# Kernel tuning notes

Hardware: AMD Instinct MI355X
Metric: run time of the kernel (lower is better)

Reference implementation:

```python
import jax, jax.numpy as jnp
import numpy as np

CONF = 0.25
IOU = 0.7
MAX_DET = 300
IMG_H = 1280
IMG_W = 1280
KPT_SHAPE = (17, 3)
MAX_NMS = 3000
BS = 16
N_ANCH = 33600  # (1280/8)^2 + (1280/16)^2 + (1280/32)^2


def setup_inputs() -> dict:
    key = jax.random.key(0)
    k1, k2, k3, k4 = jax.random.split(key, 4)
    # realistic YOLO head outputs: centers in image, positive w/h, conf in (0,1)
    cxy = jax.random.uniform(k1, (BS, 2, N_ANCH)) * jnp.array([IMG_W, IMG_H], jnp.float32).reshape(1, 2, 1)
    wh = jax.random.uniform(k2, (BS, 2, N_ANCH)) * 200.0 + 4.0
    conf = jax.random.uniform(k3, (BS, 1, N_ANCH))
    kpts = jax.random.uniform(k4, (BS, 51, N_ANCH)) * float(IMG_W)
    preds = jnp.concatenate([cxy, wh, conf, kpts], axis=1).astype(jnp.float32)
    return {"preds": preds}


def _pairwise_iou(boxes):
    # boxes: [M, 4] xyxy
    area = (boxes[:, 2] - boxes[:, 0]) * (boxes[:, 3] - boxes[:, 1])
    lt = jnp.maximum(boxes[:, None, :2], boxes[None, :, :2])
    rb = jnp.minimum(boxes[:, None, 2:], boxes[None, :, 2:])
    wh = jnp.clip(rb - lt, 0.0)
    inter = wh[..., 0] * wh[..., 1]
    return inter / (area[:, None] + area[None, :] - inter + 1e-9)


def _nms_keep(boxes, valid):
    # greedy NMS over score-descending boxes; returns bool keep mask [M]
    M = boxes.shape[0]
    idx = jnp.arange(M)
    supp = (_pairwise_iou(boxes) > IOU) & (idx[None, :] > idx[:, None])

    def body(i, keep):
        # row i suppresses later boxes only if it is itself kept
        return keep & ~(supp[i] & keep[i])

    return jax.lax.fori_loop(0, M, body, valid)


def _per_image(boxes_xywh, scores, kpts):
    # boxes_xywh: [N,4], scores: [N], kpts: [N,51]
    valid = scores > CONF
    masked = jnp.where(valid, scores, -1.0)
    order = jnp.argsort(-masked)[:MAX_NMS]  # top max_nms by score, desc
    b = boxes_xywh[order]
    sc = scores[order]
    kp = kpts[order]
    v = valid[order]
    # xywh -> xyxy with clip to image bounds
    cx, cy, w, h = b[:, 0], b[:, 1], b[:, 2], b[:, 3]
    x1 = jnp.clip(cx - w / 2, 0.0, IMG_W)
    y1 = jnp.clip(cy - h / 2, 0.0, IMG_H)
    x2 = jnp.clip(cx + w / 2, 0.0, IMG_W)
    y2 = jnp.clip(cy + h / 2, 0.0, IMG_H)
    bxy = jnp.stack([x1, y1, x2, y2], axis=-1)
    # faithful to original _clip_coords quirk: only channels 0 and 1 of the 51 clipped
    kp = kp.at[:, 0].set(jnp.clip(kp[:, 0], 0.0, IMG_W))
    kp = kp.at[:, 1].set(jnp.clip(kp[:, 1], 0.0, IMG_H))
    keep = _nms_keep(bxy, v)
    rank = jnp.cumsum(keep) - 1
    sel = keep & (rank < MAX_DET)
    tgt = jnp.where(sel, rank, MAX_DET)  # dropped rows scatter to slot MAX_DET (sliced off)
    ob = jnp.zeros((MAX_DET + 1, 4), bxy.dtype).at[tgt].set(jnp.where(sel[:, None], bxy, 0.0))[:MAX_DET]
    osc = jnp.zeros((MAX_DET + 1, 1), sc.dtype).at[tgt].set(jnp.where(sel[:, None], sc[:, None], 0.0))[:MAX_DET]
    okp = jnp.zeros((MAX_DET + 1, 51), kp.dtype).at[tgt].set(jnp.where(sel[:, None], kp, 0.0))[:MAX_DET]
    return ob, osc, okp


def reference(preds):
    bs = preds.shape[0]
    x = jnp.transpose(preds, (0, 2, 1))  # [bs, N, 56]
    ob, osc, okp = jax.vmap(_per_image)(x[..., :4], x[..., 4], x[..., 5:])
    return ob, osc, okp.reshape(bs, MAX_DET, *KPT_SHAPE)
```

## Files before the change

kernel.cpp:

```cpp
#include <hip/hip_runtime.h>
#include <stdint.h>

#define N_ANCH 33600
#define BS 16
#define NCH 56
#define MAX_NMS 3000
#define MAX_DET 300
#define CONF_T 0.25f
#define IOU_T 0.7f
#define IMG 1280.0f
#define NW 47
#define NBINS 4096
#define HIST_BINS 4097
#define CAP 4096
#define WCAP 4096
#define WC_STRIDE 16

#define OFF_CAND 0
#define OFF_WL   (OFF_CAND + BS*CAP*8)
#define OFF_WC   (OFF_WL + BS*WCAP*4)
#define OFF_KEPT (OFF_WC + BS*WC_STRIDE*4)
#define OFF_OIDX (OFF_KEPT + 64)
#define OFF_SC   (OFF_OIDX + BS*MAX_NMS*4)
#define OFF_SEL  (OFF_SC + BS*MAX_NMS*4)
#define OFF_BOX  (((OFF_SEL + BS*MAX_DET*4) + 15) & ~15)

__device__ __forceinline__ int score_bucket(float c, uint32_t* bits_out) {
    if (!(c > CONF_T)) { *bits_out = 0u; return 0; }
    uint32_t bits = __float_as_uint(c);
    *bits_out = bits;
    int bucket = (int)(bits >> 12) - 0x3E800 + 1;
    bucket = bucket < 1 ? 1 : (bucket > NBINS ? NBINS : bucket);
    return bucket;
}

__global__ void k_phase1(const float* __restrict__ preds,
                         unsigned long long* __restrict__ cand,
                         unsigned int* __restrict__ wlist, int* __restrict__ wcount,
                         int* __restrict__ oidx, float* __restrict__ sc_out,
                         float4* __restrict__ box_out) {
    __shared__ int hl[HIST_BINS];
    __shared__ int st[HIST_BINS];
    __shared__ int part[256];
    __shared__ int suf[256];
    __shared__ int ldsB, ldsM, ldsWc;
    int b = blockIdx.x, t = threadIdx.x;
    if (t == 0) { ldsWc = 0; }
    for (int i = t; i < HIST_BINS; i += 1024) hl[i] = 0;
    __syncthreads();
    const float4* conf4 = (const float4*)(preds + (size_t)b * NCH * N_ANCH + 4 * N_ANCH);
    for (int a4 = t; a4 < N_ANCH / 4; a4 += 1024) {
        float4 c4 = conf4[a4];
        uint32_t bits;
        int bk;
        bk = score_bucket(c4.x, &bits); if (bk > 0) atomicAdd(&hl[bk], 1);
        bk = score_bucket(c4.y, &bits); if (bk > 0) atomicAdd(&hl[bk], 1);
        bk = score_bucket(c4.z, &bits); if (bk > 0) atomicAdd(&hl[bk], 1);
        bk = score_bucket(c4.w, &bits); if (bk > 0) atomicAdd(&hl[bk], 1);
    }
    __syncthreads();
    if (t < 256) {
        int s = 0;
        for (int k = 0; k < 16; k++) s += hl[1 + t * 16 + k];
        part[t] = s;
    }
    __syncthreads();
    if (t == 0) {
        int run = 0;
        for (int i = 255; i >= 0; i--) { suf[i] = run; run += part[i]; }
        if (run < MAX_NMS) { ldsB = 1; ldsM = run; }
    }
    __syncthreads();
    if (t < 256) {
        int run = suf[t];
        bool maycross = (run < MAX_NMS) && (run + part[t] >= MAX_NMS);
        bool done = false;
        for (int k = 15; k >= 0; k--) {
            int bin = 1 + t * 16 + k;
            st[bin] = run;
            run += hl[bin];
            if (maycross && !done && run >= MAX_NMS) { ldsB = bin; ldsM = run; done = true; }
        }
    }
    __syncthreads();
    int B = ldsB, M = ldsM;
    if (t < 256) {
        for (int k = 0; k < 16; k++) {
            int bin = 1 + t * 16 + k;
            int c = hl[bin], s = st[bin];
            if (c > 0 && bin >= B && s < MAX_NMS) {
                int idx = atomicAdd(&ldsWc, 1);
                wlist[b * WCAP + idx] = (unsigned int)s | ((unsigned int)c << 16);
            }
        }
    }
    __syncthreads();
    for (int a4 = t; a4 < N_ANCH / 4; a4 += 1024) {
        float4 c4 = conf4[a4];
        float cv[4] = {c4.x, c4.y, c4.z, c4.w};
        #pragma unroll
        for (int q = 0; q < 4; q++) {
            uint32_t bits;
            int bucket = score_bucket(cv[q], &bits);
            if (bucket >= B && bucket > 0) {
                int pos = atomicAdd(&st[bucket], 1);
                if (pos < CAP) {
                    int a = a4 * 4 + q;
                    cand[b * CAP + pos] =
                        ((unsigned long long)bits << 32) | (uint32_t)(~(uint32_t)a);
                }
            }
        }
    }
    for (int p = M + t; p < MAX_NMS; p += 1024) {
        sc_out[b * MAX_NMS + p] = -1.0f;
        box_out[b * MAX_NMS + p] = make_float4(0.f, 0.f, 0.f, 0.f);
        oidx[b * MAX_NMS + p] = 0;
    }
    if (t == 0) wcount[b * WC_STRIDE] = ldsWc;
}

__global__ void k_rank2(const float* __restrict__ preds,
                        const unsigned long long* __restrict__ cand,
                        const unsigned int* __restrict__ wlist,
                        const int* __restrict__ wcount,
                        int* __restrict__ oidx, float* __restrict__ sc_out,
                        float4* __restrict__ box_out) {
    int b = blockIdx.x;
    int wc = wcount[b * WC_STRIDE];
    int wv = blockIdx.y * (blockDim.x >> 6) + (threadIdx.x >> 6);
    int lane = threadIdx.x & 63;
    const int wstride = gridDim.y * (blockDim.x >> 6);
    const float* pr = preds + (size_t)b * NCH * N_ANCH;
    for (int e = wv; e < wc; e += wstride) {
        unsigned int ent = wlist[b * WCAP + e];
        int s = (int)(ent & 0xffffu);
        int n = (int)(ent >> 16);
        if (s + n > CAP) n = CAP - s;
        const unsigned long long* seg = cand + b * CAP + s;
        for (int i = lane; i < n; i += 64) {
            unsigned long long ke = seg[i];
            int r = 0;
            for (int j = 0; j < n; j++) r += (seg[j] > ke);
            int pos = s + r;
            if (pos < MAX_NMS) {
                int oi = (int)(~(uint32_t)ke);
                float score = __uint_as_float((uint32_t)(ke >> 32));
                float cx = pr[0 * N_ANCH + oi], cy = pr[1 * N_ANCH + oi];
                float w  = pr[2 * N_ANCH + oi], h  = pr[3 * N_ANCH + oi];
                float4 bx;
                bx.x = fminf(fmaxf(cx - w * 0.5f, 0.f), IMG);
                bx.y = fminf(fmaxf(cy - h * 0.5f, 0.f), IMG);
                bx.z = fminf(fmaxf(cx + w * 0.5f, 0.f), IMG);
                bx.w = fminf(fmaxf(cy + h * 0.5f, 0.f), IMG);
                oidx[b * MAX_NMS + pos] = oi;
                sc_out[b * MAX_NMS + pos] = score;
                box_out[b * MAX_NMS + pos] = bx;
            }
        }
    }
}

__device__ __forceinline__ float iou_pair(float4 bi, float ai, float4 bj) {
    float aj  = (bj.z - bj.x) * (bj.w - bj.y);
    float ltx = fmaxf(bi.x, bj.x), lty = fmaxf(bi.y, bj.y);
    float rbx = fminf(bi.z, bj.z), rby = fminf(bi.w, bj.w);
    float wx  = fmaxf(rbx - ltx, 0.f), wy = fmaxf(rby - lty, 0.f);
    float inter = wx * wy;
    return inter / (ai + aj - inter + 1e-9f);
}

__device__ __forceinline__ unsigned long long readlane64(unsigned long long v, int lane) {
    uint32_t lo = (uint32_t)v, hi = (uint32_t)(v >> 32);
    uint32_t rlo = __builtin_amdgcn_readlane(lo, lane);
    uint32_t rhi = __builtin_amdgcn_readlane(hi, lane);
    return ((unsigned long long)rhi << 32) | (unsigned long long)rlo;
}

__global__ void k_nms(const float4* __restrict__ box_ws, const float* __restrict__ sc_ws,
                      int* __restrict__ sel_slot, int* __restrict__ kept_count,
                      float* __restrict__ out) {
    __shared__ float4 lbox[MAX_NMS];
    __shared__ float4 kbox[MAX_DET];
    __shared__ float  karea[MAX_DET];
    __shared__ int    lsel[MAX_DET];
    __shared__ unsigned long long pres[NW];
    __shared__ unsigned long long diag[64];
    __shared__ unsigned long long keptmask_sh;
    int b = blockIdx.x, t = threadIdx.x;
    if (t < NW) pres[t] = 0ull;
    __syncthreads();
    for (int j = t; j < MAX_NMS; j += 1024) {
        lbox[j] = box_ws[b * MAX_NMS + j];
        if (!(sc_ws[b * MAX_NMS + j] > CONF_T))
            atomicOr(&pres[j >> 6], 1ull << (j & 63));
    }
    __syncthreads();
    int kc = 0;
    for (int c = 0; c < NW && kc < MAX_DET; c++) {
        int base = c * 64;
        if (t < 64) diag[t] = 0ull;
        __syncthreads();
        {
            int jl = t >> 4, kk = t & 15;
            int j = base + jl;
            if (j < MAX_NMS && kc > 0) {
                float4 bj = lbox[j];
                bool sup = false;
                for (int kidx = kk; kidx < kc; kidx += 16) {
                    if (iou_pair(kbox[kidx], karea[kidx], bj) > IOU_T) { sup = true; break; }
                }
                if (sup) atomicOr(&pres[c], 1ull << jl);
            }
        }
        {
            int il = t >> 4;
            int j0 = (t & 15) * 4;
            int i = base + il;
            if (i < MAX_NMS) {
                float4 bi = lbox[i];
                float ai = (bi.z - bi.x) * (bi.w - bi.y);
                unsigned long long m = 0ull;
                for (int q = 0; q < 4; q++) {
                    int jl = j0 + q, j = base + jl;
                    if (j > i && j < MAX_NMS) {
                        if (iou_pair(bi, ai, lbox[j]) > IOU_T) m |= 1ull << jl;
                    }
                }
                if (m) atomicOr(&diag[il], m);
            }
        }
        __syncthreads();
        if (t < 64) {
            unsigned long long mydiag = diag[t];
            unsigned long long s = pres[c];
            unsigned long long keptm = 0ull;
            int room = MAX_DET - kc;
            int jmax = MAX_NMS - base; if (jmax > 64) jmax = 64;
            for (int bb = 0; bb < jmax; bb++) {
                if (!((s >> bb) & 1ull)) {
                    s |= readlane64(mydiag, bb);
                    keptm |= 1ull << bb;
                    if (--room == 0) break;
                }
            }
            if (t == 0) keptmask_sh = keptm;
        }
        __syncthreads();
        unsigned long long keptm = keptmask_sh;
        if (t < 64 && ((keptm >> t) & 1ull)) {
            int pos = kc + __popcll(keptm & ((1ull << t) - 1ull));
            float4 bx = lbox[base + t];
            kbox[pos] = bx;
            karea[pos] = (bx.z - bx.x) * (bx.w - bx.y);
            lsel[pos] = base + t;
        }
        kc += __popcll(keptm);
        __syncthreads();
    }
    if (t == 0) kept_count[b] = kc;
    float* ob  = out;
    float* osc = out + BS * MAX_DET * 4;
    for (int r = t; r < MAX_DET; r += 1024) {
        int det = b * MAX_DET + r;
        if (r < kc) {
            float4 bx = kbox[r];
            ob[det * 4 + 0] = bx.x; ob[det * 4 + 1] = bx.y;
            ob[det * 4 + 2] = bx.z; ob[det * 4 + 3] = bx.w;
            osc[det] = sc_ws[b * MAX_NMS + lsel[r]];
            sel_slot[b * MAX_DET + r] = lsel[r];
        } else {
            ob[det * 4 + 0] = 0.f; ob[det * 4 + 1] = 0.f;
            ob[det * 4 + 2] = 0.f; ob[det * 4 + 3] = 0.f;
            osc[det] = 0.f;
        }
    }
}

__global__ void k_kpt(const float* __restrict__ preds, const int* __restrict__ oidx_ws,
                      const int* __restrict__ sel_slot, const int* __restrict__ kept_count,
                      float* __restrict__ out) {
    int g = blockIdx.x * blockDim.x + threadIdx.x;
    int det = g >> 6, lane = g & 63;
    if (det >= BS * MAX_DET || lane >= 51) return;
    int b = det / MAX_DET, r = det - b * MAX_DET;
    float* okp = out + BS * MAX_DET * 5;
    if (r < kept_count[b]) {
        int s = sel_slot[b * MAX_DET + r];
        int oi = oidx_ws[b * MAX_NMS + s];
        float v = preds[(size_t)b * NCH * N_ANCH + (size_t)(5 + lane) * N_ANCH + oi];
        if (lane < 2) v = fminf(fmaxf(v, 0.f), IMG);
        okp[det * 51 + lane] = v;
    } else {
        okp[det * 51 + lane] = 0.f;
    }
}

extern "C" void kernel_launch(void* const* d_in, const int* in_sizes, int n_in,
                              void* d_out, int out_size, void* d_ws, size_t ws_size,
                              hipStream_t stream) {
    const float* preds = (const float*)d_in[0];
    float* out = (float*)d_out;
    char* ws = (char*)d_ws;
    unsigned long long* cand = (unsigned long long*)(ws + OFF_CAND);
    unsigned int* wlist = (unsigned int*)(ws + OFF_WL);
    int* wcount = (int*)(ws + OFF_WC);
    int* kept = (int*)(ws + OFF_KEPT);
    int* oidx = (int*)(ws + OFF_OIDX);
    float* sc = (float*)(ws + OFF_SC);
    int* sel = (int*)(ws + OFF_SEL);
    float4* box = (float4*)(ws + OFF_BOX);

    k_phase1<<<BS, 1024, 0, stream>>>(preds, cand, wlist, wcount, oidx, sc, box);
    k_rank2<<<dim3(BS, 32), 256, 0, stream>>>(preds, cand, wlist, wcount, oidx, sc, box);
    k_nms<<<BS, 1024, 0, stream>>>(box, sc, sel, kept, out);
    k_kpt<<<(BS * MAX_DET * 64 + 255) / 256, 256, 0, stream>>>(preds, oidx, sel, kept, out);
}
```

Before: 230.1 us.

## Run NMS chunk loop in a single wavefront and bound it by valid count

```diff
diff --git a/kernel.cpp b/kernel.cpp
--- a/kernel.cpp
+++ b/kernel.cpp
@@ -20,10 +20,10 @@
 #define OFF_WL   (OFF_CAND + BS*CAP*8)
 #define OFF_WC   (OFF_WL + BS*WCAP*4)
 #define OFF_KEPT (OFF_WC + BS*WC_STRIDE*4)
-#define OFF_OIDX (OFF_KEPT + 64)
+#define OFF_KOI  (OFF_KEPT + 64)
+#define OFF_OIDX (OFF_KOI + BS*MAX_DET*4)
 #define OFF_SC   (OFF_OIDX + BS*MAX_NMS*4)
-#define OFF_SEL  (OFF_SC + BS*MAX_NMS*4)
-#define OFF_BOX  (((OFF_SEL + BS*MAX_DET*4) + 15) & ~15)
+#define OFF_BOX  (((OFF_SC + BS*MAX_NMS*4) + 15) & ~15)
 
 __device__ __forceinline__ int score_bucket(float c, uint32_t* bits_out) {
     if (!(c > CONF_T)) { *bits_out = 0u; return 0; }
@@ -36,9 +36,7 @@
 
 __global__ void k_phase1(const float* __restrict__ preds,
                          unsigned long long* __restrict__ cand,
-                         unsigned int* __restrict__ wlist, int* __restrict__ wcount,
-                         int* __restrict__ oidx, float* __restrict__ sc_out,
-                         float4* __restrict__ box_out) {
+                         unsigned int* __restrict__ wlist, int* __restrict__ wcM) {
     __shared__ int hl[HIST_BINS];
     __shared__ int st[HIST_BINS];
     __shared__ int part[256];
@@ -83,7 +81,7 @@
         }
     }
     __syncthreads();
-    int B = ldsB, M = ldsM;
+    int B = ldsB;
     if (t < 256) {
         for (int k = 0; k < 16; k++) {
             int bin = 1 + t * 16 + k;
@@ -112,22 +110,17 @@
             }
         }
     }
-    for (int p = M + t; p < MAX_NMS; p += 1024) {
-        sc_out[b * MAX_NMS + p] = -1.0f;
-        box_out[b * MAX_NMS + p] = make_float4(0.f, 0.f, 0.f, 0.f);
-        oidx[b * MAX_NMS + p] = 0;
-    }
-    if (t == 0) wcount[b * WC_STRIDE] = ldsWc;
+    if (t == 0) { wcM[b * WC_STRIDE] = ldsWc; wcM[b * WC_STRIDE + 1] = ldsM; }
 }
 
 __global__ void k_rank2(const float* __restrict__ preds,
                         const unsigned long long* __restrict__ cand,
                         const unsigned int* __restrict__ wlist,
-                        const int* __restrict__ wcount,
+                        const int* __restrict__ wcM,
                         int* __restrict__ oidx, float* __restrict__ sc_out,
                         float4* __restrict__ box_out) {
     int b = blockIdx.x;
-    int wc = wcount[b * WC_STRIDE];
+    int wc = wcM[b * WC_STRIDE];
     int wv = blockIdx.y * (blockDim.x >> 6) + (threadIdx.x >> 6);
     int lane = threadIdx.x & 63;
     const int wstride = gridDim.y * (blockDim.x >> 6);
@@ -178,65 +171,43 @@
 }
 
 __global__ void k_nms(const float4* __restrict__ box_ws, const float* __restrict__ sc_ws,
-                      int* __restrict__ sel_slot, int* __restrict__ kept_count,
+                      const int* __restrict__ oidx_ws, const int* __restrict__ wcM,
+                      int* __restrict__ kept_count, int* __restrict__ koidx,
                       float* __restrict__ out) {
     __shared__ float4 lbox[MAX_NMS];
     __shared__ float4 kbox[MAX_DET];
     __shared__ float  karea[MAX_DET];
     __shared__ int    lsel[MAX_DET];
-    __shared__ unsigned long long pres[NW];
-    __shared__ unsigned long long diag[64];
-    __shared__ unsigned long long keptmask_sh;
+    __shared__ int    kc_sh;
     int b = blockIdx.x, t = threadIdx.x;
-    if (t < NW) pres[t] = 0ull;
-    __syncthreads();
-    for (int j = t; j < MAX_NMS; j += 1024) {
-        lbox[j] = box_ws[b * MAX_NMS + j];
-        if (!(sc_ws[b * MAX_NMS + j] > CONF_T))
-            atomicOr(&pres[j >> 6], 1ull << (j & 63));
-    }
-    __syncthreads();
-    int kc = 0;
-    for (int c = 0; c < NW && kc < MAX_DET; c++) {
-        int base = c * 64;
-        if (t < 64) diag[t] = 0ull;
-        __syncthreads();
-        {
-            int jl = t >> 4, kk = t & 15;
-            int j = base + jl;
-            if (j < MAX_NMS && kc > 0) {
-                float4 bj = lbox[j];
-                bool sup = false;
-                for (int kidx = kk; kidx < kc; kidx += 16) {
-                    if (iou_pair(kbox[kidx], karea[kidx], bj) > IOU_T) { sup = true; break; }
-                }
-                if (sup) atomicOr(&pres[c], 1ull << jl);
-            }
-        }
-        {
-            int il = t >> 4;
-            int j0 = (t & 15) * 4;
-            int i = base + il;
-            if (i < MAX_NMS) {
-                float4 bi = lbox[i];
-                float ai = (bi.z - bi.x) * (bi.w - bi.y);
-                unsigned long long m = 0ull;
-                for (int q = 0; q < 4; q++) {
-                    int jl = j0 + q, j = base + jl;
-                    if (j > i && j < MAX_NMS) {
-                        if (iou_pair(bi, ai, lbox[j]) > IOU_T) m |= 1ull << jl;
-                    }
-                }
-                if (m) atomicOr(&diag[il], m);
-            }
-        }
-        __syncthreads();
-        if (t < 64) {
-            unsigned long long mydiag = diag[t];
-            unsigned long long s = pres[c];
+    for (int j = t; j < MAX_NMS; j += 256) lbox[j] = box_ws[b * MAX_NMS + j];
+    __syncthreads();
+    if (t < 64) {
+        int M = wcM[b * WC_STRIDE + 1]; if (M > MAX_NMS) M = MAX_NMS;
+        int kc = 0;
+        for (int c = 0; c < NW && kc < MAX_DET; c++) {
+            int base = c * 64;
+            if (base >= M) break;
+            int j = base + t;
+            bool valid = (j < M);
+            float4 bj = lbox[valid ? j : base];
+            float aj = (bj.z - bj.x) * (bj.w - bj.y);
+            bool sup = false;
+            for (int k = 0; k < kc; k++) {
+                float4 bk = kbox[k];
+                float ak = karea[k];
+                if (valid && !sup && iou_pair(bk, ak, bj) > IOU_T) sup = true;
+            }
+            unsigned long long mydiag = 0ull;
+            int jmax = M - base; if (jmax > 64) jmax = 64;
+            for (int jl = 1; jl < jmax; jl++) {
+                float4 bjl = lbox[base + jl];
+                if (jl > t && valid && iou_pair(bj, aj, bjl) > IOU_T)
+                    mydiag |= 1ull << jl;
+            }
+            unsigned long long s = __ballot(sup || !valid);
             unsigned long long keptm = 0ull;
             int room = MAX_DET - kc;
-            int jmax = MAX_NMS - base; if (jmax > 64) jmax = 64;
             for (int bb = 0; bb < jmax; bb++) {
                 if (!((s >> bb) & 1ull)) {
                     s |= readlane64(mydiag, bb);
@@ -244,50 +215,45 @@
                     if (--room == 0) break;
                 }
             }
-            if (t == 0) keptmask_sh = keptm;
-        }
-        __syncthreads();
-        unsigned long long keptm = keptmask_sh;
-        if (t < 64 && ((keptm >> t) & 1ull)) {
-            int pos = kc + __popcll(keptm & ((1ull << t) - 1ull));
-            float4 bx = lbox[base + t];
-            kbox[pos] = bx;
-            karea[pos] = (bx.z - bx.x) * (bx.w - bx.y);
-            lsel[pos] = base + t;
-        }
-        kc += __popcll(keptm);
-        __syncthreads();
-    }
-    if (t == 0) kept_count[b] = kc;
-    float* ob  = out;
+            if ((keptm >> t) & 1ull) {
+                int pos = kc + __popcll(keptm & ((1ull << t) - 1ull));
+                kbox[pos] = bj;
+                karea[pos] = aj;
+                lsel[pos] = j;
+            }
+            __builtin_amdgcn_wave_barrier();
+            kc += __popcll(keptm);
+        }
+        if (t == 0) { kept_count[b] = kc; kc_sh = kc; }
+    }
+    __syncthreads();
+    int kc = kc_sh;
+    float4* ob = (float4*)out;
     float* osc = out + BS * MAX_DET * 4;
-    for (int r = t; r < MAX_DET; r += 1024) {
+    for (int r = t; r < MAX_DET; r += 256) {
         int det = b * MAX_DET + r;
         if (r < kc) {
-            float4 bx = kbox[r];
-            ob[det * 4 + 0] = bx.x; ob[det * 4 + 1] = bx.y;
-            ob[det * 4 + 2] = bx.z; ob[det * 4 + 3] = bx.w;
-            osc[det] = sc_ws[b * MAX_NMS + lsel[r]];
-            sel_slot[b * MAX_DET + r] = lsel[r];
+            int s = lsel[r];
+            ob[det] = kbox[r];
+            osc[det] = sc_ws[b * MAX_NMS + s];
+            koidx[det] = oidx_ws[b * MAX_NMS + s];
         } else {
-            ob[det * 4 + 0] = 0.f; ob[det * 4 + 1] = 0.f;
-            ob[det * 4 + 2] = 0.f; ob[det * 4 + 3] = 0.f;
+            ob[det] = make_float4(0.f, 0.f, 0.f, 0.f);
             osc[det] = 0.f;
-        }
-    }
-}
-
-__global__ void k_kpt(const float* __restrict__ preds, const int* __restrict__ oidx_ws,
-                      const int* __restrict__ sel_slot, const int* __restrict__ kept_count,
-                      float* __restrict__ out) {
+            koidx[det] = 0;
+        }
+    }
+}
+
+__global__ void k_kpt(const float* __restrict__ preds, const int* __restrict__ koidx,
+                      const int* __restrict__ kept_count, float* __restrict__ out) {
     int g = blockIdx.x * blockDim.x + threadIdx.x;
     int det = g >> 6, lane = g & 63;
     if (det >= BS * MAX_DET || lane >= 51) return;
     int b = det / MAX_DET, r = det - b * MAX_DET;
     float* okp = out + BS * MAX_DET * 5;
     if (r < kept_count[b]) {
-        int s = sel_slot[b * MAX_DET + r];
-        int oi = oidx_ws[b * MAX_NMS + s];
+        int oi = koidx[det];
         float v = preds[(size_t)b * NCH * N_ANCH + (size_t)(5 + lane) * N_ANCH + oi];
         if (lane < 2) v = fminf(fmaxf(v, 0.f), IMG);
         okp[det * 51 + lane] = v;
@@ -304,15 +270,15 @@
     char* ws = (char*)d_ws;
     unsigned long long* cand = (unsigned long long*)(ws + OFF_CAND);
     unsigned int* wlist = (unsigned int*)(ws + OFF_WL);
-    int* wcount = (int*)(ws + OFF_WC);
+    int* wcM = (int*)(ws + OFF_WC);
     int* kept = (int*)(ws + OFF_KEPT);
+    int* koidx = (int*)(ws + OFF_KOI);
     int* oidx = (int*)(ws + OFF_OIDX);
     float* sc = (float*)(ws + OFF_SC);
-    int* sel = (int*)(ws + OFF_SEL);
     float4* box = (float4*)(ws + OFF_BOX);
 
-    k_phase1<<<BS, 1024, 0, stream>>>(preds, cand, wlist, wcount, oidx, sc, box);
-    k_rank2<<<dim3(BS, 32), 256, 0, stream>>>(preds, cand, wlist, wcount, oidx, sc, box);
-    k_nms<<<BS, 1024, 0, stream>>>(box, sc, sel, kept, out);
-    k_kpt<<<(BS * MAX_DET * 64 + 255) / 256, 256, 0, stream>>>(preds, oidx, sel, kept, out);
-}
+    k_phase1<<<BS, 1024, 0, stream>>>(preds, cand, wlist, wcM);
+    k_rank2<<<dim3(BS, 32), 256, 0, stream>>>(preds, cand, wlist, wcM, oidx, sc, box);
+    k_nms<<<BS, 256, 0, stream>>>(box, sc, oidx, wcM, kept, koidx, out);
+    k_kpt<<<(BS * MAX_DET * 64 + 255) / 256, 256, 0, stream>>>(preds, koidx, kept, out);
+}
```

Result: slower. 333.6 us (+45.0%).
